# Kernel tuning notes

Hardware: AMD Instinct MI355X
Metric: run time of the kernel (lower is better)

Reference implementation:

```python
import jax, jax.numpy as jnp
import numpy as np

B = 4096
H = 8            # history_len
P = 13           # num_piece_types
D = 256          # d_model
NUM_TC = 8
BOARD_DIM = H * P + 1   # 105
META_DIM = H + H + 4 + 8  # 28


def setup_inputs() -> dict:
    key = jax.random.key(0)
    ks = jax.random.split(key, 16)
    inp = {
        "board_history": jax.random.randint(ks[0], (B, H, 64), 0, P, dtype=jnp.int64),
        "time_history": jax.random.uniform(ks[1], (B, H), dtype=jnp.float32),
        "rep_flags": jax.random.uniform(ks[2], (B, H), dtype=jnp.float32),
        "castling": jax.random.uniform(ks[3], (B, 4), dtype=jnp.float32),
        "ep_mask": jax.random.uniform(ks[4], (B, 64), dtype=jnp.float32),
        "scalars": jax.random.normal(ks[5], (B, 8), dtype=jnp.float32),
        "tc_cat": jax.random.randint(ks[6], (B,), 0, NUM_TC, dtype=jnp.int64),
        # learned params (torch Linear weight is (out,in); we store (in,out))
        "W_board": 0.02 * jax.random.normal(ks[7], (BOARD_DIM, D), dtype=jnp.float32),
        "W_meta": 0.001 * jax.random.normal(ks[8], (META_DIM, D), dtype=jnp.float32),
        "square_emb": jax.random.normal(ks[9], (64, D), dtype=jnp.float32),
        "square_scale": jnp.ones((64, D), dtype=jnp.float32),
        "square_bias": jnp.zeros((64, D), dtype=jnp.float32),
        "tc_table": jax.random.normal(ks[10], (NUM_TC, D), dtype=jnp.float32),
    }
    return inp


def reference(board_history, time_history, rep_flags, castling, ep_mask, scalars,
              tc_cat, W_board, W_meta, square_emb, square_scale, square_bias, tc_table):
    b = board_history.shape[0]
    # one-hot(piece_code, 13): (B, H, 64, P) -> (B, 64, H*P)
    oh = jax.nn.one_hot(board_history, P, dtype=jnp.float32)
    board_oh = jnp.transpose(oh, (0, 2, 1, 3)).reshape(b, 64, H * P)
    # board input = [one-hot history, ep flag]  -> (B, 64, 105)
    board_in = jnp.concatenate([board_oh, ep_mask[..., None]], axis=-1)
    # meta features are identical across squares; project once per batch row
    meta = jnp.concatenate([time_history, rep_flags, castling, scalars], axis=-1)  # (B, 28)
    meta_vec = meta @ W_meta  # (B, D)
    x = jnp.einsum("bsf,fd->bsd", board_in, W_board) + meta_vec[:, None, :]
    x = x + square_emb[None, :, :]
    x = x * square_scale + square_bias
    x = x + tc_table[tc_cat][:, None, :]
    return x
```

## Files before the change

### kernel.cpp

```cpp
#include <hip/hip_runtime.h>
#include <hip/hip_bf16.h>


#define D 256
#define HD 8
#define PD 13
#define NB 8
#define WB_ROWS 105
#define WB_ELEMS (WB_ROWS * D)
#define WB_F4    (WB_ELEMS / 4)

__device__ __forceinline__ unsigned short f2bf(float f) {
    unsigned int u = __float_as_uint(f);
    unsigned int r = (u + 0x7fffu + ((u >> 16) & 1u)) >> 16;
    return (unsigned short)r;
}
__device__ __forceinline__ float bf_lo(unsigned int u) { return __uint_as_float(u << 16); }
__device__ __forceinline__ float bf_hi(unsigned int u) { return __uint_as_float(u & 0xffff0000u); }

__global__ __launch_bounds__(256) void encoder_kernel(
    const int*   __restrict__ board,
    const float* __restrict__ time_h,
    const float* __restrict__ rep,
    const float* __restrict__ castl,
    const float* __restrict__ ep,
    const float* __restrict__ scal,
    const int*   __restrict__ tc_cat,
    const float* __restrict__ Wb,
    const float* __restrict__ Wm,
    const float* __restrict__ emb,
    const float* __restrict__ sscale,
    const float* __restrict__ sbias,
    const float* __restrict__ tc_tab,
    float*       __restrict__ out,
    int Btot)
{
    __shared__ __align__(16) unsigned short sWb[WB_ELEMS];
    __shared__ int   s_off[HD * 64];
    __shared__ float s_ep[64];
    __shared__ float s_meta[28];

    const int tid  = threadIdx.x;
    const int wave = tid >> 6;
    const int lane = tid & 63;
    const int d    = lane * 4;

    for (int i = tid; i < WB_F4; i += 256) {
        const float4 w = *(const float4*)(Wb + i * 4);
        uint2 pk;
        pk.x = (unsigned int)f2bf(w.x) | ((unsigned int)f2bf(w.y) << 16);
        pk.y = (unsigned int)f2bf(w.z) | ((unsigned int)f2bf(w.w) << 16);
        *(uint2*)(&sWb[i * 4]) = pk;
    }

    const float4 w104 = *(const float4*)(&Wb[104 * D + d]);

    const int b0 = blockIdx.x * NB;
    const int nb = min(NB, Btot - b0);

    for (int bi = 0; bi < nb; ++bi) {
        const int b = b0 + bi;

        __syncthreads();

        {
            int e = tid;
            #pragma unroll
            for (int r = 0; r < 2; ++r, e += 256) {
                const int p = board[b * 512 + e];
                s_off[e] = ((e >> 6) * PD + p) * (D * 2);
            }
        }
        if (tid < 64) s_ep[tid] = ep[b * 64 + tid];
        if (tid < 8)        s_meta[tid] = time_h[b * 8 + tid];
        else if (tid < 16)  s_meta[tid] = rep[b * 8 + (tid - 8)];
        else if (tid < 20)  s_meta[tid] = castl[b * 4 + (tid - 16)];
        else if (tid < 28)  s_meta[tid] = scal[b * 8 + (tid - 20)];

        __syncthreads();

        float4 mv = make_float4(0.f, 0.f, 0.f, 0.f);
        #pragma unroll
        for (int f = 0; f < 28; ++f) {
            const float  m = s_meta[f];
            const float4 w = *(const float4*)(&Wm[f * D + d]);
            mv.x = fmaf(m, w.x, mv.x);
            mv.y = fmaf(m, w.y, mv.y);
            mv.z = fmaf(m, w.z, mv.z);
            mv.w = fmaf(m, w.w, mv.w);
        }
        const int tcc = tc_cat[b];
        const float4 tc4 = *(const float4*)(&tc_tab[tcc * D + d]);

        const size_t outb = (size_t)b * 64 * D;
        const char* wb_base = (const char*)sWb + (size_t)lane * 8;

        #pragma unroll 4
        for (int i = 0; i < 16; ++i) {
            const int s = wave * 16 + i;
            float4 acc = mv;
            #pragma unroll
            for (int h = 0; h < HD; ++h) {
                const int ro = s_off[h * 64 + s];
                const uint2 u = *(const uint2*)(wb_base + ro);
                acc.x += bf_lo(u.x);
                acc.y += bf_hi(u.x);
                acc.z += bf_lo(u.y);
                acc.w += bf_hi(u.y);
            }
            const float epv = s_ep[s];
            acc.x = fmaf(epv, w104.x, acc.x);
            acc.y = fmaf(epv, w104.y, acc.y);
            acc.z = fmaf(epv, w104.z, acc.z);
            acc.w = fmaf(epv, w104.w, acc.w);

            const float4 e  = *(const float4*)(&emb[s * D + d]);
            const float4 sc = *(const float4*)(&sscale[s * D + d]);
            const float4 bi4 = *(const float4*)(&sbias[s * D + d]);

            float4 x;
            x.x = fmaf(acc.x + e.x, sc.x, bi4.x) + tc4.x;
            x.y = fmaf(acc.y + e.y, sc.y, bi4.y) + tc4.y;
            x.z = fmaf(acc.z + e.z, sc.z, bi4.z) + tc4.z;
            x.w = fmaf(acc.w + e.w, sc.w, bi4.w) + tc4.w;

            *(float4*)(&out[outb + s * D + d]) = x;
        }
    }
}

extern "C" void kernel_launch(void* const* d_in, const int* in_sizes, int n_in,
                              void* d_out, int out_size, void* d_ws, size_t ws_size,
                              hipStream_t stream) {
    const int*   board  = (const int*)  d_in[0];
    const float* time_h = (const float*)d_in[1];
    const float* rep    = (const float*)d_in[2];
    const float* castl  = (const float*)d_in[3];
    const float* ep     = (const float*)d_in[4];
    const float* scal   = (const float*)d_in[5];
    const int*   tc_cat = (const int*)  d_in[6];
    const float* Wb     = (const float*)d_in[7];
    const float* Wm     = (const float*)d_in[8];
    const float* emb    = (const float*)d_in[9];
    const float* sscale = (const float*)d_in[10];
    const float* sbias  = (const float*)d_in[11];
    const float* tc_tab = (const float*)d_in[12];
    float* out = (float*)d_out;

    const int B = in_sizes[6];
    const int grid = (B + NB - 1) / NB;
    encoder_kernel<<<grid, 256, 0, stream>>>(board, time_h, rep, castl, ep, scal,
                                             tc_cat, Wb, Wm, emb, sscale, sbias,
                                             tc_tab, out, B);
}
```

Baseline: 370.9 us.

## Assign batch rows per wave, broadcast board codes via shuffles, drop per-row barriers

```diff
diff --git a/kernel.cpp b/kernel.cpp
--- a/kernel.cpp
+++ b/kernel.cpp
@@ -5,15 +5,15 @@
 #define D 256
 #define HD 8
 #define PD 13
-#define NB 8
+#define ROWS_PER_WAVE 2
+#define ROWS_PER_BLOCK 8
 #define WB_ROWS 105
 #define WB_ELEMS (WB_ROWS * D)
 #define WB_F4    (WB_ELEMS / 4)
 
 __device__ __forceinline__ unsigned short f2bf(float f) {
     unsigned int u = __float_as_uint(f);
-    unsigned int r = (u + 0x7fffu + ((u >> 16) & 1u)) >> 16;
-    return (unsigned short)r;
+    return (unsigned short)((u + 0x7fffu + ((u >> 16) & 1u)) >> 16);
 }
 __device__ __forceinline__ float bf_lo(unsigned int u) { return __uint_as_float(u << 16); }
 __device__ __forceinline__ float bf_hi(unsigned int u) { return __uint_as_float(u & 0xffff0000u); }
@@ -36,9 +36,6 @@
     int Btot)
 {
     __shared__ __align__(16) unsigned short sWb[WB_ELEMS];
-    __shared__ int   s_off[HD * 64];
-    __shared__ float s_ep[64];
-    __shared__ float s_meta[28];
 
     const int tid  = threadIdx.x;
     const int wave = tid >> 6;
@@ -55,76 +52,94 @@
 
     const float4 w104 = *(const float4*)(&Wb[104 * D + d]);
 
-    const int b0 = blockIdx.x * NB;
-    const int nb = min(NB, Btot - b0);
+    __syncthreads();
 
-    for (int bi = 0; bi < nb; ++bi) {
-        const int b = b0 + bi;
+    const int b_base = blockIdx.x * ROWS_PER_BLOCK + wave * ROWS_PER_WAVE;
 
-        __syncthreads();
+    int    bh[ROWS_PER_WAVE][HD];
+    float  epr[ROWS_PER_WAVE];
+    float4 mv[ROWS_PER_WAVE];
+    float4 tc[ROWS_PER_WAVE];
+    bool   valid[ROWS_PER_WAVE];
 
-        {
-            int e = tid;
-            #pragma unroll
-            for (int r = 0; r < 2; ++r, e += 256) {
-                const int p = board[b * 512 + e];
-                s_off[e] = ((e >> 6) * PD + p) * (D * 2);
-            }
+    #pragma unroll
+    for (int r = 0; r < ROWS_PER_WAVE; ++r) {
+        const int b = b_base + r;
+        valid[r] = (b < Btot);
+        const int bc = valid[r] ? b : 0;
+
+        #pragma unroll
+        for (int h = 0; h < HD; ++h)
+            bh[r][h] = board[bc * 512 + h * 64 + lane];
+        epr[r] = ep[bc * 64 + lane];
+
+        float4 m = make_float4(0.f, 0.f, 0.f, 0.f);
+        #pragma unroll
+        for (int f = 0; f < 8; ++f) {
+            const float  c = time_h[bc * 8 + f];
+            const float4 w = *(const float4*)(&Wm[f * D + d]);
+            m.x = fmaf(c, w.x, m.x); m.y = fmaf(c, w.y, m.y);
+            m.z = fmaf(c, w.z, m.z); m.w = fmaf(c, w.w, m.w);
         }
-        if (tid < 64) s_ep[tid] = ep[b * 64 + tid];
-        if (tid < 8)        s_meta[tid] = time_h[b * 8 + tid];
-        else if (tid < 16)  s_meta[tid] = rep[b * 8 + (tid - 8)];
-        else if (tid < 20)  s_meta[tid] = castl[b * 4 + (tid - 16)];
-        else if (tid < 28)  s_meta[tid] = scal[b * 8 + (tid - 20)];
+        #pragma unroll
+        for (int f = 0; f < 8; ++f) {
+            const float  c = rep[bc * 8 + f];
+            const float4 w = *(const float4*)(&Wm[(8 + f) * D + d]);
+            m.x = fmaf(c, w.x, m.x); m.y = fmaf(c, w.y, m.y);
+            m.z = fmaf(c, w.z, m.z); m.w = fmaf(c, w.w, m.w);
+        }
+        #pragma unroll
+        for (int f = 0; f < 4; ++f) {
+            const float  c = castl[bc * 4 + f];
+            const float4 w = *(const float4*)(&Wm[(16 + f) * D + d]);
+            m.x = fmaf(c, w.x, m.x); m.y = fmaf(c, w.y, m.y);
+            m.z = fmaf(c, w.z, m.z); m.w = fmaf(c, w.w, m.w);
+        }
+        #pragma unroll
+        for (int f = 0; f < 8; ++f) {
+            const float  c = scal[bc * 8 + f];
+            const float4 w = *(const float4*)(&Wm[(20 + f) * D + d]);
+            m.x = fmaf(c, w.x, m.x); m.y = fmaf(c, w.y, m.y);
+            m.z = fmaf(c, w.z, m.z); m.w = fmaf(c, w.w, m.w);
+        }
+        mv[r] = m;
+        tc[r] = *(const float4*)(&tc_tab[tc_cat[bc] * D + d]);
+    }
 
-        __syncthreads();
+    const char* wb_lane = (const char*)sWb + (size_t)lane * 8;
 
-        float4 mv = make_float4(0.f, 0.f, 0.f, 0.f);
+    #pragma unroll 2
+    for (int s = 0; s < 64; ++s) {
+        const float4 e  = *(const float4*)(&emb[s * D + d]);
+        const float4 sc = *(const float4*)(&sscale[s * D + d]);
+        const float4 bi = *(const float4*)(&sbias[s * D + d]);
+
         #pragma unroll
-        for (int f = 0; f < 28; ++f) {
-            const float  m = s_meta[f];
-            const float4 w = *(const float4*)(&Wm[f * D + d]);
-            mv.x = fmaf(m, w.x, mv.x);
-            mv.y = fmaf(m, w.y, mv.y);
-            mv.z = fmaf(m, w.z, mv.z);
-            mv.w = fmaf(m, w.w, mv.w);
-        }
-        const int tcc = tc_cat[b];
-        const float4 tc4 = *(const float4*)(&tc_tab[tcc * D + d]);
-
-        const size_t outb = (size_t)b * 64 * D;
-        const char* wb_base = (const char*)sWb + (size_t)lane * 8;
-
-        #pragma unroll 4
-        for (int i = 0; i < 16; ++i) {
-            const int s = wave * 16 + i;
-            float4 acc = mv;
+        for (int r = 0; r < ROWS_PER_WAVE; ++r) {
+            if (!valid[r]) continue;
+            float4 acc = mv[r];
             #pragma unroll
             for (int h = 0; h < HD; ++h) {
-                const int ro = s_off[h * 64 + s];
-                const uint2 u = *(const uint2*)(wb_base + ro);
+                const int p = __shfl(bh[r][h], s, 64);
+                const uint2 u = *(const uint2*)(wb_lane + (h * PD + p) * (D * 2));
                 acc.x += bf_lo(u.x);
                 acc.y += bf_hi(u.x);
                 acc.z += bf_lo(u.y);
                 acc.w += bf_hi(u.y);
             }
-            const float epv = s_ep[s];
+            const float epv = __shfl(epr[r], s, 64);
             acc.x = fmaf(epv, w104.x, acc.x);
             acc.y = fmaf(epv, w104.y, acc.y);
             acc.z = fmaf(epv, w104.z, acc.z);
             acc.w = fmaf(epv, w104.w, acc.w);
 
-            const float4 e  = *(const float4*)(&emb[s * D + d]);
-            const float4 sc = *(const float4*)(&sscale[s * D + d]);
-            const float4 bi4 = *(const float4*)(&sbias[s * D + d]);
+            float4 x;
+            x.x = fmaf(acc.x + e.x, sc.x, bi.x) + tc[r].x;
+            x.y = fmaf(acc.y + e.y, sc.y, bi.y) + tc[r].y;
+            x.z = fmaf(acc.z + e.z, sc.z, bi.z) + tc[r].z;
+            x.w = fmaf(acc.w + e.w, sc.w, bi.w) + tc[r].w;
 
-            float4 x;
-            x.x = fmaf(acc.x + e.x, sc.x, bi4.x) + tc4.x;
-            x.y = fmaf(acc.y + e.y, sc.y, bi4.y) + tc4.y;
-            x.z = fmaf(acc.z + e.z, sc.z, bi4.z) + tc4.z;
-            x.w = fmaf(acc.w + e.w, sc.w, bi4.w) + tc4.w;
-
-            *(float4*)(&out[outb + s * D + d]) = x;
+            *(float4*)(&out[(size_t)(b_base + r) * 64 * D + s * D + d]) = x;
         }
     }
 }
@@ -148,7 +163,7 @@
     float* out = (float*)d_out;
 
     const int B = in_sizes[6];
-    const int grid = (B + NB - 1) / NB;
+    const int grid = (B + ROWS_PER_BLOCK - 1) / ROWS_PER_BLOCK;
     encoder_kernel<<<grid, 256, 0, stream>>>(board, time_h, rep, castl, ep, scal,
                                              tc_cat, Wb, Wm, emb, sscale, sbias,
                                              tc_tab, out, B);
```

Measured after the change: 350.2 us. 5.6% less time.
